# Performance work log

Hardware: AMD Instinct MI355X
Metric: run time of the kernel (lower is better)

The kernel has to match this reference:

```python
import jax, jax.numpy as jnp
import numpy as np

NUM_HEADS = 12


def setup_inputs() -> dict:
    key = jax.random.key(0)
    ks = jax.random.split(key, 6)
    B, H, W, C = 8, 32, 32, 768
    hd = C // NUM_HEADS
    n = lambda k, shp, sc: jax.random.normal(k, shp, dtype=jnp.float32) * sc
    return {
        "x": n(ks[0], (B, H, W, C), 1.0),
        "qkv_w": n(ks[1], (3 * C, C), 0.02),
        "qkv_b": jnp.zeros((3 * C,), jnp.float32),
        "proj_w": n(ks[2], (C, C), 0.02),
        "proj_b": jnp.zeros((C,), jnp.float32),
        "rel_pos_h": n(ks[3], (2 * H - 1, hd), 0.02),
        "rel_pos_w": n(ks[4], (2 * W - 1, hd), 0.02),
    }


def reference(x, qkv_w, qkv_b, proj_w, proj_b, rel_pos_h, rel_pos_w):
    B, H, W, C = x.shape
    nH = NUM_HEADS
    hd = C // nH
    scale = hd ** -0.5
    # qkv projection (torch Linear convention: y = x @ W.T + b)
    qkv = x.reshape(B, H * W, C) @ qkv_w.T + qkv_b              # (B, HW, 3C)
    qkv = qkv.reshape(B, H * W, 3, nH, hd).transpose(2, 0, 3, 1, 4)
    qkv = qkv.reshape(3, B * nH, H * W, hd)
    q, k, v = qkv[0], qkv[1], qkv[2]
    attn = jnp.einsum('bqd,bkd->bqk', q * scale, k)             # (B*nH, HW, HW)
    # decomposed relative position bias (q_size == k_size, so no interpolation)
    coords_h = jnp.arange(H)[:, None] - jnp.arange(H)[None, :] + (H - 1)
    coords_w = jnp.arange(W)[:, None] - jnp.arange(W)[None, :] + (W - 1)
    Rh = rel_pos_h[coords_h]                                    # (H, H, hd)
    Rw = rel_pos_w[coords_w]                                    # (W, W, hd)
    r_q = q.reshape(B * nH, H, W, hd)
    rel_h = jnp.einsum('bhwc,hkc->bhwk', r_q, Rh)               # (B*nH, H, W, H)
    rel_w = jnp.einsum('bhwc,wkc->bhwk', r_q, Rw)               # (B*nH, H, W, W)
    attn = (attn.reshape(B * nH, H, W, H, W)
            + rel_h[..., :, None] + rel_w[..., None, :]).reshape(B * nH, H * W, H * W)
    attn = jax.nn.softmax(attn, axis=-1)
    out = attn @ v                                              # (B*nH, HW, hd)
    out = out.reshape(B, nH, H, W, hd).transpose(0, 2, 3, 1, 4).reshape(B, H, W, C)
    return out @ proj_w.T + proj_b
```

## Files before the change

### kernel.cpp

```cpp
#include <hip/hip_runtime.h>

using u16 = unsigned short;
using u32 = unsigned int;
typedef __attribute__((ext_vector_type(8))) short bf16x8;
typedef __attribute__((ext_vector_type(4))) float f32x4;

__device__ __forceinline__ float bf2f(u32 h) {
  union { u32 u; float f; } c; c.u = h << 16; return c.f;
}
__device__ __forceinline__ u16 f2bf(float f) {
  union { float f; u32 u; } c; c.f = f;
  u32 u = c.u;
  u32 r = (u + 0x7FFFu + ((u >> 16) & 1u)) >> 16;
  return (u16)r;
}

#define GLD16(gsrc, ldst)                                                      \
  __builtin_amdgcn_global_load_lds(                                            \
      (const __attribute__((address_space(1))) unsigned int*)(gsrc),           \
      (__attribute__((address_space(3))) unsigned int*)(ldst), 16, 0, 0)

__device__ __forceinline__ int kappa(int ss) {
  return (ss & 0x23) | ((ss & 0x10) >> 2) | ((ss & 0x0C) << 1);
}

__global__ void cvt_kernel(const float* __restrict__ src, u16* __restrict__ dst, int n) {
  int i = (blockIdx.x * blockDim.x + threadIdx.x) * 4;
  if (i < n) {
    float4 v = *(const float4*)(src + i);
    ushort4 o;
    o.x = f2bf(v.x); o.y = f2bf(v.y); o.z = f2bf(v.z); o.w = f2bf(v.w);
    *(ushort4*)(dst + i) = o;
  }
}

__global__ void tbl_kernel(const float* __restrict__ rph, const float* __restrict__ rpw,
                           u16* __restrict__ tbl) {
  int i = blockIdx.x * 256 + threadIdx.x;
  int row = i >> 6, d = i & 63;
  float v = 0.f;
  if (row < 63) v = rph[row * 64 + d];
  else if (row >= 64 && row < 127) v = rpw[(row - 64) * 64 + d];
  tbl[i] = f2bf(v * 1.44269504f);
}

__global__ __launch_bounds__(256, 2) void pgemm_kernel(
    const u16* __restrict__ A, const u16* __restrict__ tbl, u16* __restrict__ P) {
  __shared__ u16 As[128 * 64];
  __shared__ u16 Bs[128 * 64];
  const int tid = threadIdx.x;
  const int lane = tid & 63, wave = tid >> 6;
  const int lr = lane & 15, lg = lane >> 4;
  const int m0 = blockIdx.x * 128;
  const int wm = (wave >> 1) * 64, wn = (wave & 1) * 64;

#pragma unroll
  for (int i = 0; i < 4; ++i) {
    int c = tid + i * 256;
    int row = c >> 3, pp = c & 7;
    int pl = pp ^ (row & 7);
    GLD16(A + (size_t)(m0 + row) * 64 + pl * 8, &As[c * 8]);
    GLD16(tbl + row * 64 + pl * 8, &Bs[c * 8]);
  }
  __syncthreads();

  bf16x8 a[4][2], b[4][2];
#pragma unroll
  for (int m = 0; m < 4; ++m) {
    int row = wm + m * 16 + lr;
#pragma unroll
    for (int kf = 0; kf < 2; ++kf)
      a[m][kf] = *(const bf16x8*)&As[(row * 64 + kf * 32 + lg * 8) ^ ((row & 7) << 3)];
  }
#pragma unroll
  for (int n = 0; n < 4; ++n) {
    int row = wn + n * 16 + lr;
#pragma unroll
    for (int kf = 0; kf < 2; ++kf)
      b[n][kf] = *(const bf16x8*)&Bs[(row * 64 + kf * 32 + lg * 8) ^ ((row & 7) << 3)];
  }

  f32x4 acc[4][4] = {};
#pragma unroll
  for (int kf = 0; kf < 2; ++kf)
#pragma unroll
    for (int m = 0; m < 4; ++m)
#pragma unroll
      for (int n = 0; n < 4; ++n)
        acc[m][n] = __builtin_amdgcn_mfma_f32_16x16x32_bf16(a[m][kf], b[n][kf], acc[m][n], 0, 0, 0);

#pragma unroll
  for (int m = 0; m < 4; ++m)
#pragma unroll
    for (int n = 0; n < 4; ++n) {
      const int col = wn + n * 16 + lr;
#pragma unroll
      for (int r = 0; r < 4; ++r) {
        const int g = m0 + wm + m * 16 + lg * 4 + r;
        const int s = g & 1023;
        const int hq = s >> 5, w = s & 31;
        u16 hv = f2bf(acc[m][n][r]);
        if (col < 64) {
          int kh = hq + 31 - col;
          if ((unsigned)kh < 32u) P[(size_t)g * 64 + 32 + kh] = hv;
        } else {
          int kw = w + 95 - col;
          if ((unsigned)kw < 32u) P[(size_t)g * 64 + kw] = hv;
        }
      }
    }
}

template <int MODE>
__global__ __launch_bounds__(512, 2) void gemm128(
    const u16* __restrict__ A, const u16* __restrict__ B,
    const float* __restrict__ bias, u16* __restrict__ oq, u16* __restrict__ ok,
    u16* __restrict__ ovt, float* __restrict__ ofp) {
  __shared__ u16 As[2][128 * 64];
  __shared__ u16 Bs[2][128 * 64];
  const int tid = threadIdx.x;
  const int lane = tid & 63, wave = tid >> 6;
  const int lr = lane & 15, lg = lane >> 4;

  const int nbx = (MODE == 0) ? 18 : 6;
  const int nwg = nbx * 64;
  int id = blockIdx.y * nbx + blockIdx.x;
  int nid = (id & 7) * (nwg >> 3) + (id >> 3);
  const int m0 = (nid / nbx) * 128, n0 = (nid % nbx) * 128;
  const int wm = (wave >> 2) * 64, wn = (wave & 3) * 32;

  f32x4 acc[4][2] = {};

  const u16* ap[2];
  const u16* bp[2];
#pragma unroll
  for (int i = 0; i < 2; ++i) {
    int c = tid + i * 512;
    int row = c >> 3, pp = c & 7;
    int pl = pp ^ (row & 7);
    if constexpr (MODE == 0) {
      ap[i] = A + (size_t)(m0 + row) * 768 + pl * 8;
    } else {
      int g = m0 + row;
      ap[i] = A + ((size_t)((g >> 10) * 12) << 16) + (g & 1023) * 64 + pl * 8;
    }
    bp[i] = B + (size_t)(n0 + row) * 768 + pl * 8;
  }
  constexpr int dA = (MODE == 0) ? 64 : 65536;

  auto stage = [&](int bi) {
#pragma unroll
    for (int i = 0; i < 2; ++i) {
      int c = tid + i * 512;
      GLD16(ap[i], &As[bi][c * 8]);
      GLD16(bp[i], &Bs[bi][c * 8]);
      ap[i] += dA;
      bp[i] += 64;
    }
  };

  stage(0);
#pragma unroll 1
  for (int t = 0; t < 12; ++t) {
    const int cur = t & 1;
    if (t < 11) {
      stage(cur ^ 1);
      asm volatile("s_waitcnt vmcnt(4)" ::: "memory");
    } else {
      asm volatile("s_waitcnt vmcnt(0)" ::: "memory");
    }
    __builtin_amdgcn_sched_barrier(0);
    __builtin_amdgcn_s_barrier();
    __builtin_amdgcn_sched_barrier(0);

    bf16x8 a[4][2], b[2][2];
#pragma unroll
    for (int m = 0; m < 4; ++m) {
      int row = wm + m * 16 + lr;
#pragma unroll
      for (int kf = 0; kf < 2; ++kf)
        a[m][kf] = *(const bf16x8*)&As[cur][(row * 64 + kf * 32 + lg * 8) ^ ((row & 7) << 3)];
    }
#pragma unroll
    for (int n = 0; n < 2; ++n) {
      int row = wn + n * 16 + lr;
#pragma unroll
      for (int kf = 0; kf < 2; ++kf)
        b[n][kf] = *(const bf16x8*)&Bs[cur][(row * 64 + kf * 32 + lg * 8) ^ ((row & 7) << 3)];
    }
    __builtin_amdgcn_s_setprio(1);
#pragma unroll
    for (int kf = 0; kf < 2; ++kf)
#pragma unroll
      for (int m = 0; m < 4; ++m)
#pragma unroll
        for (int n = 0; n < 2; ++n)
          acc[m][n] = __builtin_amdgcn_mfma_f32_16x16x32_bf16(a[m][kf], b[n][kf], acc[m][n], 0, 0, 0);
    __builtin_amdgcn_s_setprio(0);

    __builtin_amdgcn_sched_barrier(0);
    __builtin_amdgcn_s_barrier();
    __builtin_amdgcn_sched_barrier(0);
  }

#pragma unroll
  for (int m = 0; m < 4; ++m) {
    const int grow0 = m0 + wm + m * 16 + lg * 4;
#pragma unroll
    for (int n = 0; n < 2; ++n) {
      const int gcol = n0 + wn + n * 16 + lr;
      const float bv = bias[gcol];
      if constexpr (MODE == 0) {
        int which = (gcol >= 1536) ? 2 : (gcol >= 768 ? 1 : 0);
        int rem = gcol - which * 768;
        int bh = (grow0 >> 10) * 12 + (rem >> 6);
        if (which == 2) {
          int s0 = grow0 & 1023;
          int colb = (s0 & ~63) | kappa(s0 & 63);
          ushort4 pk;
          pk.x = f2bf(acc[m][n][0] + bv);
          pk.y = f2bf(acc[m][n][1] + bv);
          pk.z = f2bf(acc[m][n][2] + bv);
          pk.w = f2bf(acc[m][n][3] + bv);
          *(ushort4*)&ovt[((size_t)bh << 16) + (size_t)(rem & 63) * 1024 + colb] = pk;
        } else {
          u16* dst = (which == 0) ? oq : ok;
#pragma unroll
          for (int r = 0; r < 4; ++r) {
            int s = (grow0 & 1023) + r;
            dst[((size_t)bh << 16) + s * 64 + (rem & 63)] = f2bf(acc[m][n][r] + bv);
          }
        }
      } else {
#pragma unroll
        for (int r = 0; r < 4; ++r)
          ofp[(size_t)(grow0 + r) * 768 + gcol] = acc[m][n][r] + bv;
      }
    }
  }
}

__global__ __launch_bounds__(256, 2) void attn_kernel(
    const u16* __restrict__ qb, const u16* __restrict__ kb,
    const u16* __restrict__ vtb, const u16* __restrict__ pb,
    u16* __restrict__ ao) {
  __shared__ u16 Ks[2][64 * 64];
  __shared__ u16 Vs[2][64 * 64];

  const int tid = threadIdx.x;
  const int lane = tid & 63, wave = tid >> 6;
  const int lr = lane & 15, lg = lane >> 4;
  const int bh = blockIdx.x;
  const int q0 = blockIdx.y * 128 + wave * 32;
  const size_t hb = (size_t)bh << 16;

  bf16x8 qf[2][2];
#pragma unroll
  for (int m = 0; m < 2; ++m)
#pragma unroll
    for (int kf = 0; kf < 2; ++kf)
      qf[m][kf] = *(const bf16x8*)(qb + hb + (size_t)(q0 + m * 16 + lr) * 64 + kf * 32 + lg * 8);

  u32 Wh[2][16];
  float rwv[2][2][4];
#pragma unroll
  for (int m = 0; m < 2; ++m) {
    int g = q0 + m * 16 + lr;
    const u16* sb = pb + (((size_t)bh << 10) + g) * 64;
    const uint4* s4 = (const uint4*)(sb + 32);
    uint4 ha = s4[0], hc = s4[1], he = s4[2], hg = s4[3];
    Wh[m][0] = ha.x;  Wh[m][1] = ha.y;  Wh[m][2] = ha.z;  Wh[m][3] = ha.w;
    Wh[m][4] = hc.x;  Wh[m][5] = hc.y;  Wh[m][6] = hc.z;  Wh[m][7] = hc.w;
    Wh[m][8] = he.x;  Wh[m][9] = he.y;  Wh[m][10] = he.z; Wh[m][11] = he.w;
    Wh[m][12] = hg.x; Wh[m][13] = hg.y; Wh[m][14] = hg.z; Wh[m][15] = hg.w;
    uint2 u0 = *(const uint2*)(sb + lg * 4);
    uint2 u1 = *(const uint2*)(sb + 16 + lg * 4);
    rwv[m][0][0] = bf2f(u0.x & 0xffffu); rwv[m][0][1] = bf2f(u0.x >> 16);
    rwv[m][0][2] = bf2f(u0.y & 0xffffu); rwv[m][0][3] = bf2f(u0.y >> 16);
    rwv[m][1][0] = bf2f(u1.x & 0xffffu); rwv[m][1][1] = bf2f(u1.x >> 16);
    rwv[m][1][2] = bf2f(u1.y & 0xffffu); rwv[m][1][3] = bf2f(u1.y >> 16);
  }

  float lsum[2] = {};
  f32x4 acco[2][4] = {};

  const u16* kp[2];
  const u16* vp[2];
#pragma unroll
  for (int i = 0; i < 2; ++i) {
    int c = tid + i * 256;
    int row = c >> 3, pp = c & 7;
    int pl = pp ^ (row & 7);
    kp[i] = kb + hb + (size_t)row * 64 + pl * 8;
    vp[i] = vtb + hb + (size_t)row * 1024 + pl * 8;
  }

  auto stage = [&](int bi) {
#pragma unroll
    for (int i = 0; i < 2; ++i) {
      int c = tid + i * 256;
      GLD16(kp[i], &Ks[bi][c * 8]);
      GLD16(vp[i], &Vs[bi][c * 8]);
      kp[i] += 4096;
      vp[i] += 64;
    }
  };

  stage(0);

  const float scale2 = 0.125f * 1.44269504f;

#pragma unroll 1
  for (int t = 0; t < 16; ++t) {
    const int cur = t & 1;
    if (t < 15) {
      stage(cur ^ 1);
      asm volatile("s_waitcnt vmcnt(4)" ::: "memory");
    } else {
      asm volatile("s_waitcnt vmcnt(0)" ::: "memory");
    }
    __builtin_amdgcn_sched_barrier(0);
    __builtin_amdgcn_s_barrier();
    __builtin_amdgcn_sched_barrier(0);

    f32x4 sac[2][4] = {};
    __builtin_amdgcn_s_setprio(1);
#pragma unroll
    for (int kf = 0; kf < 2; ++kf) {
#pragma unroll
      for (int f = 0; f < 4; ++f) {
        int row = f * 16 + lr;
        bf16x8 kv = *(const bf16x8*)&Ks[cur][(row * 64 + kf * 32 + lg * 8) ^ ((row & 7) << 3)];
#pragma unroll
        for (int m = 0; m < 2; ++m)
          sac[m][f] = __builtin_amdgcn_mfma_f32_16x16x32_bf16(kv, qf[m][kf], sac[m][f], 0, 0, 0);
      }
    }
    __builtin_amdgcn_s_setprio(0);

    bf16x8 paf[2][2];
#pragma unroll
    for (int m = 0; m < 2; ++m) {
      u32 wrd = Wh[m][0];
      float c0 = bf2f(wrd & 0xffffu);
      float c1 = bf2f(wrd >> 16);
      float bs[2][2][4];
#pragma unroll
      for (int i = 0; i < 2; ++i)
#pragma unroll
        for (int r = 0; r < 4; ++r) {
          bs[0][i][r] = c0 + rwv[m][i][r];
          bs[1][i][r] = c1 + rwv[m][i][r];
        }
      union { u32 w[4]; bf16x8 v; } wa, wb;
#pragma unroll
      for (int f = 0; f < 4; ++f) {
        const int j = (f >> 1) & 1, i = f & 1;
        float p0 = __builtin_amdgcn_exp2f(sac[m][f][0] * scale2 + bs[j][i][0]);
        float p1 = __builtin_amdgcn_exp2f(sac[m][f][1] * scale2 + bs[j][i][1]);
        float p2 = __builtin_amdgcn_exp2f(sac[m][f][2] * scale2 + bs[j][i][2]);
        float p3 = __builtin_amdgcn_exp2f(sac[m][f][3] * scale2 + bs[j][i][3]);
        lsum[m] += (p0 + p1) + (p2 + p3);
        u32 w0, w1;
        asm("v_cvt_pk_bf16_f32 %0, %1, %2" : "=v"(w0) : "v"(p0), "v"(p1));
        asm("v_cvt_pk_bf16_f32 %0, %1, %2" : "=v"(w1) : "v"(p2), "v"(p3));
        if (f < 2) { wa.w[f * 2] = w0; wa.w[f * 2 + 1] = w1; }
        else       { wb.w[(f - 2) * 2] = w0; wb.w[(f - 2) * 2 + 1] = w1; }
      }
      paf[m][0] = wa.v;
      paf[m][1] = wb.v;
    }

#pragma unroll
    for (int k = 0; k < 15; ++k) { Wh[0][k] = Wh[0][k + 1]; Wh[1][k] = Wh[1][k + 1]; }

    __builtin_amdgcn_s_setprio(1);
#pragma unroll
    for (int kf = 0; kf < 2; ++kf) {
#pragma unroll
      for (int fd = 0; fd < 4; ++fd) {
        int drow = fd * 16 + lr;
        bf16x8 vv = *(const bf16x8*)&Vs[cur][(drow * 64 + kf * 32 + lg * 8) ^ ((drow & 7) << 3)];
#pragma unroll
        for (int m = 0; m < 2; ++m)
          acco[m][fd] = __builtin_amdgcn_mfma_f32_16x16x32_bf16(paf[m][kf], vv, acco[m][fd], 0, 0, 0);
      }
    }
    __builtin_amdgcn_s_setprio(0);

    __builtin_amdgcn_sched_barrier(0);
    __builtin_amdgcn_s_barrier();
    __builtin_amdgcn_sched_barrier(0);
  }

#pragma unroll
  for (int m = 0; m < 2; ++m) {
    float s = lsum[m];
    s += __shfl_xor(s, 16);
    s += __shfl_xor(s, 32);
    float inv = 1.0f / s;
#pragma unroll
    for (int r = 0; r < 4; ++r) {
      int src = (lane & 48) + ((lane & 48) >> 2) + r;
      float invr = __shfl(inv, src);
      int gq = q0 + m * 16 + lg * 4 + r;
#pragma unroll
      for (int fd = 0; fd < 4; ++fd)
        ao[hb + (size_t)gq * 64 + fd * 16 + lr] = f2bf(acco[m][fd][r] * invr);
    }
  }
}

extern "C" void kernel_launch(void* const* d_in, const int* in_sizes, int n_in,
                              void* d_out, int out_size, void* d_ws, size_t ws_size,
                              hipStream_t stream) {
  const float* x = (const float*)d_in[0];
  const float* qkv_w = (const float*)d_in[1];
  const float* qkv_b = (const float*)d_in[2];
  const float* proj_w = (const float*)d_in[3];
  const float* proj_b = (const float*)d_in[4];
  const float* rel_pos_h = (const float*)d_in[5];
  const float* rel_pos_w = (const float*)d_in[6];
  float* out = (float*)d_out;

  char* ws = (char*)d_ws;
  u16* x_bf = (u16*)(ws + 0);
  u16* qkvw_bf = (u16*)(ws + 12582912);
  u16* projw_bf = (u16*)(ws + 16121856);
  u16* qbuf = (u16*)(ws + 17301504);
  u16* kbuf = (u16*)(ws + 29884416);
  u16* vtbuf = (u16*)(ws + 42467328);
  u16* pbuf = (u16*)(ws + 55050240);
  u16* tbl = (u16*)(ws + 80216064);
  u16* aobuf = x_bf;

  cvt_kernel<<<6144, 256, 0, stream>>>(x, x_bf, 6291456);
  cvt_kernel<<<1728, 256, 0, stream>>>(qkv_w, qkvw_bf, 1769472);
  cvt_kernel<<<576, 256, 0, stream>>>(proj_w, projw_bf, 589824);
  tbl_kernel<<<32, 256, 0, stream>>>(rel_pos_h, rel_pos_w, tbl);

  gemm128<0><<<dim3(18, 64), 512, 0, stream>>>(x_bf, qkvw_bf, qkv_b, qbuf, kbuf, vtbuf, nullptr);

  pgemm_kernel<<<768, 256, 0, stream>>>(qbuf, tbl, pbuf);

  attn_kernel<<<dim3(96, 8), 256, 0, stream>>>(qbuf, kbuf, vtbuf, pbuf, aobuf);

  gemm128<1><<<dim3(6, 64), 512, 0, stream>>>(aobuf, projw_bf, proj_b, nullptr, nullptr, nullptr, out);
}
```

Measured before the change: 135.1 us.

## Fold relative position bias into augmented Q/K dot product of width 128

Result: faster. 130.5 us (-3.4%).

```diff
diff --git a/kernel.cpp b/kernel.cpp
--- a/kernel.cpp
+++ b/kernel.cpp
@@ -41,11 +41,26 @@
   float v = 0.f;
   if (row < 63) v = rph[row * 64 + d];
   else if (row >= 64 && row < 127) v = rpw[(row - 64) * 64 + d];
-  tbl[i] = f2bf(v * 1.44269504f);
+  tbl[i] = f2bf(v * 8.0f);
+}
+
+__global__ void aug_kernel(u16* __restrict__ kb) {
+  int j = blockIdx.x * 256 + threadIdx.x;
+  int g = j >> 4, q4 = j & 15;
+  int s = g & 1023;
+  int d0 = 64 + q4 * 4;
+  int kwslot = 64 + (s & 31);
+  int khslot = 96 + (s >> 5);
+  ushort4 v;
+  v.x = (d0 == kwslot || d0 == khslot) ? 0x3F80 : 0;
+  v.y = (d0 + 1 == kwslot || d0 + 1 == khslot) ? 0x3F80 : 0;
+  v.z = (d0 + 2 == kwslot || d0 + 2 == khslot) ? 0x3F80 : 0;
+  v.w = (d0 + 3 == kwslot || d0 + 3 == khslot) ? 0x3F80 : 0;
+  *(ushort4*)&kb[(size_t)g * 128 + d0] = v;
 }
 
 __global__ __launch_bounds__(256, 2) void pgemm_kernel(
-    const u16* __restrict__ A, const u16* __restrict__ tbl, u16* __restrict__ P) {
+    const u16* __restrict__ A, const u16* __restrict__ tbl, u16* __restrict__ Q2) {
   __shared__ u16 As[128 * 64];
   __shared__ u16 Bs[128 * 64];
   const int tid = threadIdx.x;
@@ -59,7 +74,7 @@
     int c = tid + i * 256;
     int row = c >> 3, pp = c & 7;
     int pl = pp ^ (row & 7);
-    GLD16(A + (size_t)(m0 + row) * 64 + pl * 8, &As[c * 8]);
+    GLD16(A + (size_t)(m0 + row) * 128 + pl * 8, &As[c * 8]);
     GLD16(tbl + row * 64 + pl * 8, &Bs[c * 8]);
   }
   __syncthreads();
@@ -102,10 +117,10 @@
         u16 hv = f2bf(acc[m][n][r]);
         if (col < 64) {
           int kh = hq + 31 - col;
-          if ((unsigned)kh < 32u) P[(size_t)g * 64 + 32 + kh] = hv;
+          if ((unsigned)kh < 32u) Q2[(size_t)g * 128 + 96 + kh] = hv;
         } else {
           int kw = w + 95 - col;
-          if ((unsigned)kw < 32u) P[(size_t)g * 64 + kw] = hv;
+          if ((unsigned)kw < 32u) Q2[(size_t)g * 128 + 64 + kw] = hv;
         }
       }
     }
@@ -225,10 +240,11 @@
           *(ushort4*)&ovt[((size_t)bh << 16) + (size_t)(rem & 63) * 1024 + colb] = pk;
         } else {
           u16* dst = (which == 0) ? oq : ok;
+          const float sc = (which == 0) ? 0.18033688f : 1.0f;
 #pragma unroll
           for (int r = 0; r < 4; ++r) {
             int s = (grow0 & 1023) + r;
-            dst[((size_t)bh << 16) + s * 64 + (rem & 63)] = f2bf(acc[m][n][r] + bv);
+            dst[((size_t)bh << 17) + s * 128 + (rem & 63)] = f2bf((acc[m][n][r] + bv) * sc);
           }
         }
       } else {
@@ -242,80 +258,68 @@
 
 __global__ __launch_bounds__(256, 2) void attn_kernel(
     const u16* __restrict__ qb, const u16* __restrict__ kb,
-    const u16* __restrict__ vtb, const u16* __restrict__ pb,
-    u16* __restrict__ ao) {
-  __shared__ u16 Ks[2][64 * 64];
-  __shared__ u16 Vs[2][64 * 64];
+    const u16* __restrict__ vtb, u16* __restrict__ ao) {
+  __shared__ u16 Ks[2][8192];
+  __shared__ u16 Vs[2][4096];
 
   const int tid = threadIdx.x;
   const int lane = tid & 63, wave = tid >> 6;
   const int lr = lane & 15, lg = lane >> 4;
   const int bh = blockIdx.x;
   const int q0 = blockIdx.y * 128 + wave * 32;
-  const size_t hb = (size_t)bh << 16;
-
-  bf16x8 qf[2][2];
+  const size_t hb2 = (size_t)bh << 17;
+  const size_t hbv = (size_t)bh << 16;
+
+  bf16x8 qf[2][4];
 #pragma unroll
   for (int m = 0; m < 2; ++m)
 #pragma unroll
-    for (int kf = 0; kf < 2; ++kf)
-      qf[m][kf] = *(const bf16x8*)(qb + hb + (size_t)(q0 + m * 16 + lr) * 64 + kf * 32 + lg * 8);
-
-  u32 Wh[2][16];
-  float rwv[2][2][4];
-#pragma unroll
-  for (int m = 0; m < 2; ++m) {
-    int g = q0 + m * 16 + lr;
-    const u16* sb = pb + (((size_t)bh << 10) + g) * 64;
-    const uint4* s4 = (const uint4*)(sb + 32);
-    uint4 ha = s4[0], hc = s4[1], he = s4[2], hg = s4[3];
-    Wh[m][0] = ha.x;  Wh[m][1] = ha.y;  Wh[m][2] = ha.z;  Wh[m][3] = ha.w;
-    Wh[m][4] = hc.x;  Wh[m][5] = hc.y;  Wh[m][6] = hc.z;  Wh[m][7] = hc.w;
-    Wh[m][8] = he.x;  Wh[m][9] = he.y;  Wh[m][10] = he.z; Wh[m][11] = he.w;
-    Wh[m][12] = hg.x; Wh[m][13] = hg.y; Wh[m][14] = hg.z; Wh[m][15] = hg.w;
-    uint2 u0 = *(const uint2*)(sb + lg * 4);
-    uint2 u1 = *(const uint2*)(sb + 16 + lg * 4);
-    rwv[m][0][0] = bf2f(u0.x & 0xffffu); rwv[m][0][1] = bf2f(u0.x >> 16);
-    rwv[m][0][2] = bf2f(u0.y & 0xffffu); rwv[m][0][3] = bf2f(u0.y >> 16);
-    rwv[m][1][0] = bf2f(u1.x & 0xffffu); rwv[m][1][1] = bf2f(u1.x >> 16);
-    rwv[m][1][2] = bf2f(u1.y & 0xffffu); rwv[m][1][3] = bf2f(u1.y >> 16);
-  }
+    for (int kf = 0; kf < 4; ++kf)
+      qf[m][kf] = *(const bf16x8*)(qb + hb2 + (size_t)(q0 + m * 16 + lr) * 128 + kf * 32 + lg * 8);
 
   float lsum[2] = {};
   f32x4 acco[2][4] = {};
 
-  const u16* kp[2];
+  const u16* kp[4];
   const u16* vp[2];
+#pragma unroll
+  for (int i = 0; i < 4; ++i) {
+    int c = tid + i * 256;
+    int half = c >> 9, row = (c >> 3) & 63, pp = c & 7;
+    int pl = pp ^ (row & 7);
+    kp[i] = kb + hb2 + (size_t)row * 128 + half * 64 + pl * 8;
+  }
 #pragma unroll
   for (int i = 0; i < 2; ++i) {
     int c = tid + i * 256;
     int row = c >> 3, pp = c & 7;
     int pl = pp ^ (row & 7);
-    kp[i] = kb + hb + (size_t)row * 64 + pl * 8;
-    vp[i] = vtb + hb + (size_t)row * 1024 + pl * 8;
+    vp[i] = vtb + hbv + (size_t)row * 1024 + pl * 8;
   }
 
   auto stage = [&](int bi) {
+#pragma unroll
+    for (int i = 0; i < 4; ++i) {
+      int c = tid + i * 256;
+      GLD16(kp[i], &Ks[bi][c * 8]);
+      kp[i] += 8192;
+    }
 #pragma unroll
     for (int i = 0; i < 2; ++i) {
       int c = tid + i * 256;
-      GLD16(kp[i], &Ks[bi][c * 8]);
       GLD16(vp[i], &Vs[bi][c * 8]);
-      kp[i] += 4096;
       vp[i] += 64;
     }
   };
 
   stage(0);
-
-  const float scale2 = 0.125f * 1.44269504f;
 
 #pragma unroll 1
   for (int t = 0; t < 16; ++t) {
     const int cur = t & 1;
     if (t < 15) {
       stage(cur ^ 1);
-      asm volatile("s_waitcnt vmcnt(4)" ::: "memory");
+      asm volatile("s_waitcnt vmcnt(6)" ::: "memory");
     } else {
       asm volatile("s_waitcnt vmcnt(0)" ::: "memory");
     }
@@ -326,11 +330,13 @@
     f32x4 sac[2][4] = {};
     __builtin_amdgcn_s_setprio(1);
 #pragma unroll
-    for (int kf = 0; kf < 2; ++kf) {
+    for (int kf = 0; kf < 4; ++kf) {
+      const int half = kf >> 1, kfl = kf & 1;
 #pragma unroll
       for (int f = 0; f < 4; ++f) {
         int row = f * 16 + lr;
-        bf16x8 kv = *(const bf16x8*)&Ks[cur][(row * 64 + kf * 32 + lg * 8) ^ ((row & 7) << 3)];
+        bf16x8 kv = *(const bf16x8*)&Ks[cur][half * 4096 +
+            ((row * 64 + kfl * 32 + lg * 8) ^ ((row & 7) << 3))];
 #pragma unroll
         for (int m = 0; m < 2; ++m)
           sac[m][f] = __builtin_amdgcn_mfma_f32_16x16x32_bf16(kv, qf[m][kf], sac[m][f], 0, 0, 0);
@@ -341,25 +347,13 @@
     bf16x8 paf[2][2];
 #pragma unroll
     for (int m = 0; m < 2; ++m) {
-      u32 wrd = Wh[m][0];
-      float c0 = bf2f(wrd & 0xffffu);
-      float c1 = bf2f(wrd >> 16);
-      float bs[2][2][4];
-#pragma unroll
-      for (int i = 0; i < 2; ++i)
-#pragma unroll
-        for (int r = 0; r < 4; ++r) {
-          bs[0][i][r] = c0 + rwv[m][i][r];
-          bs[1][i][r] = c1 + rwv[m][i][r];
-        }
       union { u32 w[4]; bf16x8 v; } wa, wb;
 #pragma unroll
       for (int f = 0; f < 4; ++f) {
-        const int j = (f >> 1) & 1, i = f & 1;
-        float p0 = __builtin_amdgcn_exp2f(sac[m][f][0] * scale2 + bs[j][i][0]);
-        float p1 = __builtin_amdgcn_exp2f(sac[m][f][1] * scale2 + bs[j][i][1]);
-        float p2 = __builtin_amdgcn_exp2f(sac[m][f][2] * scale2 + bs[j][i][2]);
-        float p3 = __builtin_amdgcn_exp2f(sac[m][f][3] * scale2 + bs[j][i][3]);
+        float p0 = __builtin_amdgcn_exp2f(sac[m][f][0]);
+        float p1 = __builtin_amdgcn_exp2f(sac[m][f][1]);
+        float p2 = __builtin_amdgcn_exp2f(sac[m][f][2]);
+        float p3 = __builtin_amdgcn_exp2f(sac[m][f][3]);
         lsum[m] += (p0 + p1) + (p2 + p3);
         u32 w0, w1;
         asm("v_cvt_pk_bf16_f32 %0, %1, %2" : "=v"(w0) : "v"(p0), "v"(p1));
@@ -371,9 +365,6 @@
       paf[m][1] = wb.v;
     }
 
-#pragma unroll
-    for (int k = 0; k < 15; ++k) { Wh[0][k] = Wh[0][k + 1]; Wh[1][k] = Wh[1][k + 1]; }
-
     __builtin_amdgcn_s_setprio(1);
 #pragma unroll
     for (int kf = 0; kf < 2; ++kf) {
@@ -406,7 +397,7 @@
       int gq = q0 + m * 16 + lg * 4 + r;
 #pragma unroll
       for (int fd = 0; fd < 4; ++fd)
-        ao[hb + (size_t)gq * 64 + fd * 16 + lr] = f2bf(acco[m][fd][r] * invr);
+        ao[hbv + (size_t)gq * 64 + fd * 16 + lr] = f2bf(acco[m][fd][r] * invr);
     }
   }
 }
@@ -427,10 +418,9 @@
   u16* x_bf = (u16*)(ws + 0);
   u16* qkvw_bf = (u16*)(ws + 12582912);
   u16* projw_bf = (u16*)(ws + 16121856);
-  u16* qbuf = (u16*)(ws + 17301504);
-  u16* kbuf = (u16*)(ws + 29884416);
-  u16* vtbuf = (u16*)(ws + 42467328);
-  u16* pbuf = (u16*)(ws + 55050240);
+  u16* qbuf2 = (u16*)(ws + 17301504);
+  u16* kbuf2 = (u16*)(ws + 42467328);
+  u16* vtbuf = (u16*)(ws + 67633152);
   u16* tbl = (u16*)(ws + 80216064);
   u16* aobuf = x_bf;
 
@@ -438,12 +428,13 @@
   cvt_kernel<<<1728, 256, 0, stream>>>(qkv_w, qkvw_bf, 1769472);
   cvt_kernel<<<576, 256, 0, stream>>>(proj_w, projw_bf, 589824);
   tbl_kernel<<<32, 256, 0, stream>>>(rel_pos_h, rel_pos_w, tbl);
-
-  gemm128<0><<<dim3(18, 64), 512, 0, stream>>>(x_bf, qkvw_bf, qkv_b, qbuf, kbuf, vtbuf, nullptr);
-
-  pgemm_kernel<<<768, 256, 0, stream>>>(qbuf, tbl, pbuf);
-
-  attn_kernel<<<dim3(96, 8), 256, 0, stream>>>(qbuf, kbuf, vtbuf, pbuf, aobuf);
+  aug_kernel<<<6144, 256, 0, stream>>>(kbuf2);
+
+  gemm128<0><<<dim3(18, 64), 512, 0, stream>>>(x_bf, qkvw_bf, qkv_b, qbuf2, kbuf2, vtbuf, nullptr);
+
+  pgemm_kernel<<<768, 256, 0, stream>>>(qbuf2, tbl, qbuf2);
+
+  attn_kernel<<<dim3(96, 8), 256, 0, stream>>>(qbuf2, kbuf2, vtbuf, aobuf);
 
   gemm128<1><<<dim3(6, 64), 512, 0, stream>>>(aobuf, projw_bf, proj_b, nullptr, nullptr, nullptr, out);
 }
```
